# Optimization experiments

Measured on AMD Instinct MI355X. Metric: run time of the kernel, lower is better.

The kernel has to match this reference:

```python
import jax, jax.numpy as jnp
import numpy as np

DIM = 768      # d_model = d_inner (expand=1)
BSZ = 4
SEQ = 2048
DS  = 8        # d_state
DR  = 48       # dt_rank = ceil(768/16)
DC  = 4        # d_conv
EPS = 1e-5


def setup_inputs() -> dict:
    key = jax.random.key(0)
    ks = jax.random.split(key, 16)
    g = lambda k, shape, s=0.02: (jax.random.normal(k, shape, jnp.float32) * s)
    A_init = jnp.log(jnp.tile(jnp.arange(1, DS + 1, dtype=jnp.float32), (DIM, 1)))  # (D, N)
    return {
        "x": jax.random.normal(ks[0], (BSZ, SEQ, DIM), jnp.float32),
        "ln_g": jnp.ones((DIM,), jnp.float32),
        "ln_b": jnp.zeros((DIM,), jnp.float32),
        "in_proj_w": g(ks[1], (2 * DIM, DIM)),
        "conv_w": g(ks[2], (DIM, 1, DC), 0.2),
        "conv_b": jnp.zeros((DIM,), jnp.float32),
        "x_proj_w": g(ks[3], (DR + 2 * DS, DIM)),
        "dt_proj_w": g(ks[4], (DIM, DR), 0.1),
        "dt_proj_b": g(ks[5], (DIM,), 0.5) - 4.0,  # softplus -> small positive dt
        "A_log": A_init,
        "D": jnp.ones((DIM,), jnp.float32),
        "conv_w_b": g(ks[6], (DIM, 1, DC), 0.2),
        "conv_b_b": jnp.zeros((DIM,), jnp.float32),
        "x_proj_w_b": g(ks[7], (DR + 2 * DS, DIM)),
        "dt_proj_w_b": g(ks[8], (DIM, DR), 0.1),
        "dt_proj_b_b": g(ks[9], (DIM,), 0.5) - 4.0,
        "A_b_log": A_init,
        "D_b": jnp.ones((DIM,), jnp.float32),
        "out_proj_w": g(ks[10], (DIM, DIM)),
    }


def _ssm_dir(xl, zl, conv_w, conv_b, x_proj_w, dt_proj_w, dt_proj_b, A_log, Dp):
    # xl, zl: (B, L, D)
    d = xl.shape[-1]
    # causal depthwise conv along L (pad left d_conv-1)
    xc = jnp.pad(xl, ((0, 0), (DC - 1, 0), (0, 0))).transpose(0, 2, 1)  # (B, D, L+3)
    xconv = jax.lax.conv_general_dilated(
        xc, conv_w, (1,), "VALID", feature_group_count=d,
        dimension_numbers=("NCH", "OIH", "NCH"))  # (B, D, L)
    xs = jax.nn.silu(xconv + conv_b[None, :, None]).transpose(0, 2, 1)  # (B, L, D)
    x_dbl = xs @ x_proj_w.T                              # (B, L, R+2N)
    dt, Bm, Cm = jnp.split(x_dbl, [DR, DR + DS], axis=-1)
    delta = jax.nn.softplus(dt @ dt_proj_w.T + dt_proj_b)  # (B, L, D)
    A = -jnp.exp(A_log)                                  # (D, N)
    dA = jnp.exp(delta[..., None] * A)                   # (B, L, D, N)
    dBx = delta[..., None] * Bm[:, :, None, :] * xs[..., None]

    def comb(c1, c2):
        a1, b1 = c1
        a2, b2 = c2
        return (a2 * a1, a2 * b1 + b2)

    _, h = jax.lax.associative_scan(comb, (dA, dBx), axis=1)  # (B, L, D, N)
    y = jnp.einsum("bldn,bln->bld", h, Cm) + xs * Dp
    return y * jax.nn.silu(zl)


def _forward(x, ln_g, ln_b, in_proj_w, conv_w, conv_b, x_proj_w, dt_proj_w,
             dt_proj_b, A_log, D, conv_w_b, conv_b_b, x_proj_w_b, dt_proj_w_b,
             dt_proj_b_b, A_b_log, D_b, out_proj_w):
    mu = x.mean(-1, keepdims=True)
    var = ((x - mu) ** 2).mean(-1, keepdims=True)
    xn = (x - mu) * jax.lax.rsqrt(var + EPS) * ln_g + ln_b
    xz = xn @ in_proj_w.T                      # (B, L, 2D)
    xf, zf = jnp.split(xz, 2, axis=-1)
    # forward-direction scan
    yf = _ssm_dir(xf, zf, conv_w, conv_b, x_proj_w, dt_proj_w, dt_proj_b, A_log, D)
    # backward-direction scan (flip seq, scan, flip back) -- bimamba v2
    yb = _ssm_dir(xf[:, ::-1], zf[:, ::-1], conv_w_b, conv_b_b, x_proj_w_b,
                  dt_proj_w_b, dt_proj_b_b, A_b_log, D_b)[:, ::-1]
    out = ((yf + yb) * 0.5) @ out_proj_w.T     # if_devide_out=True
    return out + x                              # residual skip


def reference(x, ln_g, ln_b, in_proj_w, conv_w, conv_b, x_proj_w, dt_proj_w,
              dt_proj_b, A_log, D, conv_w_b, conv_b_b, x_proj_w_b, dt_proj_w_b,
              dt_proj_b_b, A_b_log, D_b, out_proj_w):
    return _forward(x, ln_g, ln_b, in_proj_w, conv_w, conv_b, x_proj_w,
                    dt_proj_w, dt_proj_b, A_log, D, conv_w_b, conv_b_b,
                    x_proj_w_b, dt_proj_w_b, dt_proj_b_b, A_b_log, D_b,
                    out_proj_w)
```

## Files before the change

### kernel.cpp

```cpp
#include <hip/hip_runtime.h>

#define Bsz 4
#define Lseq 2048
#define Dm 768
#define BL (Bsz * Lseq)
#define DS 8
#define DR 48
#define NCH 64
#define CHL 32
#define CW 32

typedef short bf16x8 __attribute__((ext_vector_type(8)));
typedef float f32x4 __attribute__((ext_vector_type(4)));
typedef float f32x2 __attribute__((ext_vector_type(2)));

typedef __attribute__((address_space(1))) const void gvoid_t;
typedef __attribute__((address_space(3))) void lvoid_t;
__device__ __forceinline__ void gll16(const void* g, void* l) {
    __builtin_amdgcn_global_load_lds((gvoid_t*)g, (lvoid_t*)l, 16, 0, 0);
}

__device__ __forceinline__ ushort f2bf(float f) {
    unsigned u = __builtin_bit_cast(unsigned, f);
    u += 0x7fff + ((u >> 16) & 1);
    return (ushort)(u >> 16);
}
__device__ __forceinline__ float bf2f(ushort u) {
    return __builtin_bit_cast(float, ((unsigned)u) << 16);
}
__device__ __forceinline__ float fsilu(float x) { return x / (1.f + __expf(-x)); }
__device__ __forceinline__ float fsoftplus(float x) {
    return fmaxf(x, 0.f) + __logf(1.f + __expf(-fabsf(x)));
}

#define PN0 (2 * Dm * Dm)
#define PN1 (Dm * Dm)
#define PN2 (64 * Dm)
#define PN5 (Dm * 64)
#define PREP_N (PN0 + PN1 + 2 * PN2 + 2 * PN5)
#define PREP_BLOCKS ((PREP_N + 255) / 256)

__global__ __launch_bounds__(256) void ln_prep_k(const float* __restrict__ x,
                                                 const float* __restrict__ g,
                                                 const float* __restrict__ bta,
                                                 ushort* __restrict__ xn,
                                                 const float* __restrict__ inW,
                                                 const float* __restrict__ outW,
                                                 const float* __restrict__ xpW,
                                                 const float* __restrict__ xpWb,
                                                 const float* __restrict__ dtw,
                                                 const float* __restrict__ dtwb,
                                                 ushort* __restrict__ w_in,
                                                 ushort* __restrict__ w_out,
                                                 ushort* __restrict__ w_xp,
                                                 ushort* __restrict__ w_xpb,
                                                 ushort* __restrict__ dtp,
                                                 ushort* __restrict__ dtpb) {
    if (blockIdx.x >= BL) {
        int i = (blockIdx.x - BL) * 256 + threadIdx.x;
        if (i < PN0) { w_in[i] = f2bf(inW[i]); return; }
        i -= PN0;
        if (i < PN1) { w_out[i] = f2bf(outW[i]); return; }
        i -= PN1;
        if (i < PN2) { w_xp[i] = f2bf(xpW[i]); return; }
        i -= PN2;
        if (i < PN2) { w_xpb[i] = f2bf(xpWb[i]); return; }
        i -= PN2;
        if (i < PN5) { int d = i >> 6, k = i & 63; dtp[i] = (k < DR) ? f2bf(dtw[d * DR + k]) : (ushort)0; return; }
        i -= PN5;
        if (i < PN5) { int d = i >> 6, k = i & 63; dtpb[i] = (k < DR) ? f2bf(dtwb[d * DR + k]) : (ushort)0; return; }
        return;
    }
    const int row = blockIdx.x, t = threadIdx.x;
    const float* xr = x + (size_t)row * Dm;
    float v0 = xr[t], v1 = xr[t + 256], v2 = xr[t + 512];
    float s1 = v0 + v1 + v2;
    float s2 = v0 * v0 + v1 * v1 + v2 * v2;
    for (int o = 32; o > 0; o >>= 1) { s1 += __shfl_down(s1, o); s2 += __shfl_down(s2, o); }
    __shared__ float r1[4], r2[4];
    int wv = t >> 6;
    if ((t & 63) == 0) { r1[wv] = s1; r2[wv] = s2; }
    __syncthreads();
    s1 = r1[0] + r1[1] + r1[2] + r1[3];
    s2 = r2[0] + r2[1] + r2[2] + r2[3];
    float mu = s1 * (1.f / Dm);
    float var = s2 * (1.f / Dm) - mu * mu;
    float rs = rsqrtf(var + 1e-5f);
    ushort* o = xn + (size_t)row * Dm;
    o[t]       = f2bf((v0 - mu) * rs * g[t]       + bta[t]);
    o[t + 256] = f2bf((v1 - mu) * rs * g[t + 256] + bta[t + 256]);
    o[t + 512] = f2bf((v2 - mu) * rs * g[t + 512] + bta[t + 512]);
}

template <int OUT_BF16, int ADD_RES>
__global__ __launch_bounds__(256) void gemm128(const ushort* __restrict__ A,
                                               const ushort* __restrict__ B,
                                               const float* __restrict__ res,
                                               void* __restrict__ Cout,
                                               int M, int N, int K) {
    __shared__ __align__(16) ushort lA[128 * 64];
    __shared__ __align__(16) ushort lB[128 * 64];
    const int t = threadIdx.x;
    const int nwgx = gridDim.x;
    const int nwg = nwgx * gridDim.y;
    const int orig = blockIdx.y * nwgx + blockIdx.x;
    const int cpx = nwg >> 3;
    const int swz = (orig & 7) * cpx + (orig >> 3);
    const int bm = swz % nwgx, bn = swz / nwgx;
    const int wave = t >> 6, lane = t & 63;
    const int wm = wave >> 1, wn = wave & 1;
    f32x4 acc[4][4] = {};

    const int lrow = lane >> 3;
    const int scol = ((lane & 7) ^ lrow) * 8;
    const int srow = wave * 32 + lrow;
    const ushort* gA = A + (size_t)(bm * 128 + srow) * K + scol;
    const ushort* gB = B + (size_t)(bn * 128 + srow) * K + scol;
    ushort* sA = &lA[srow * 64 + (lane & 7) * 8];
    ushort* sB = &lB[srow * 64 + (lane & 7) * 8];

    const int fr = lane & 15;
    const int fg = lane >> 4;
    const int rx = fr & 7;

    for (int k0 = 0; k0 < K; k0 += 64) {
#pragma unroll
        for (int j = 0; j < 4; j++) {
            gll16(gA + (size_t)(j * 8) * K, sA + j * 8 * 64);
            gll16(gB + (size_t)(j * 8) * K, sB + j * 8 * 64);
        }
        gA += 64; gB += 64;
        __syncthreads();
        bf16x8 af0[4], bf0[4], af1[4], bf1[4];
#pragma unroll
        for (int mi = 0; mi < 4; mi++) {
            int row = wm * 64 + mi * 16 + fr;
            af0[mi] = *(const bf16x8*)&lA[row * 64 + ((fg ^ rx) * 8)];
            af1[mi] = *(const bf16x8*)&lA[row * 64 + (((4 + fg) ^ rx) * 8)];
        }
#pragma unroll
        for (int ni = 0; ni < 4; ni++) {
            int row = wn * 64 + ni * 16 + fr;
            bf0[ni] = *(const bf16x8*)&lB[row * 64 + ((fg ^ rx) * 8)];
            bf1[ni] = *(const bf16x8*)&lB[row * 64 + (((4 + fg) ^ rx) * 8)];
        }
#pragma unroll
        for (int mi = 0; mi < 4; mi++)
#pragma unroll
            for (int ni = 0; ni < 4; ni++) {
                acc[mi][ni] = __builtin_amdgcn_mfma_f32_16x16x32_bf16(
                    af0[mi], bf0[ni], acc[mi][ni], 0, 0, 0);
                acc[mi][ni] = __builtin_amdgcn_mfma_f32_16x16x32_bf16(
                    af1[mi], bf1[ni], acc[mi][ni], 0, 0, 0);
            }
        __syncthreads();
    }
    const int rb = fg * 4;
#pragma unroll
    for (int mi = 0; mi < 4; mi++)
#pragma unroll
        for (int ni = 0; ni < 4; ni++) {
            int col = bn * 128 + wn * 64 + ni * 16 + fr;
#pragma unroll
            for (int r = 0; r < 4; r++) {
                int row = bm * 128 + wm * 64 + mi * 16 + rb + r;
                size_t o = (size_t)row * N + col;
                float v = acc[mi][ni][r];
                if (OUT_BF16) {
                    ((ushort*)Cout)[o] = f2bf(v);
                } else {
                    if (ADD_RES) v += res[o];
                    ((float*)Cout)[o] = v;
                }
            }
        }
}

__global__ __launch_bounds__(256) void gemm_dt(const ushort* __restrict__ A,
                                               const ushort* __restrict__ Bp0,
                                               const ushort* __restrict__ Bp1,
                                               const float* __restrict__ bias0,
                                               const float* __restrict__ bias1,
                                               ushort* __restrict__ delta) {
    __shared__ __align__(16) ushort lA[128 * 64];
    __shared__ __align__(16) ushort lB[128 * 64];
    const int t = threadIdx.x;
    const int nwgx = gridDim.x;
    const int nwg = nwgx * gridDim.y;
    const int orig = blockIdx.y * nwgx + blockIdx.x;
    const int cpx = nwg >> 3;
    const int swz = (orig & 7) * cpx + (orig >> 3);
    const int bm = swz % nwgx, bn = swz / nwgx;
    const ushort* __restrict__ B = (bm < BL / 128) ? Bp0 : Bp1;
    const float* __restrict__ bias = (bm < BL / 128) ? bias0 : bias1;
    const int wave = t >> 6, lane = t & 63;
    const int wm = wave >> 1, wn = wave & 1;
    f32x4 acc[4][4] = {};

    const int lrow = lane >> 3;
    const int scol = ((lane & 7) ^ lrow) * 8;
    const int srow = wave * 32 + lrow;
    const ushort* gA = A + (size_t)(bm * 128 + srow) * 64 + scol;
    const ushort* gB = B + (size_t)(bn * 128 + srow) * 64 + scol;
    ushort* sA = &lA[srow * 64 + (lane & 7) * 8];
    ushort* sB = &lB[srow * 64 + (lane & 7) * 8];

    const int fr = lane & 15;
    const int fg = lane >> 4;
    const int rx = fr & 7;

#pragma unroll
    for (int j = 0; j < 4; j++) {
        gll16(gA + (size_t)(j * 8) * 64, sA + j * 8 * 64);
        gll16(gB + (size_t)(j * 8) * 64, sB + j * 8 * 64);
    }
    __syncthreads();
    {
        bf16x8 af0[4], bf0[4], af1[4], bf1[4];
#pragma unroll
        for (int mi = 0; mi < 4; mi++) {
            int row = wm * 64 + mi * 16 + fr;
            af0[mi] = *(const bf16x8*)&lA[row * 64 + ((fg ^ rx) * 8)];
            af1[mi] = *(const bf16x8*)&lA[row * 64 + (((4 + fg) ^ rx) * 8)];
        }
#pragma unroll
        for (int ni = 0; ni < 4; ni++) {
            int row = wn * 64 + ni * 16 + fr;
            bf0[ni] = *(const bf16x8*)&lB[row * 64 + ((fg ^ rx) * 8)];
            bf1[ni] = *(const bf16x8*)&lB[row * 64 + (((4 + fg) ^ rx) * 8)];
        }
#pragma unroll
        for (int mi = 0; mi < 4; mi++)
#pragma unroll
            for (int ni = 0; ni < 4; ni++) {
                acc[mi][ni] = __builtin_amdgcn_mfma_f32_16x16x32_bf16(
                    af0[mi], bf0[ni], acc[mi][ni], 0, 0, 0);
                acc[mi][ni] = __builtin_amdgcn_mfma_f32_16x16x32_bf16(
                    af1[mi], bf1[ni], acc[mi][ni], 0, 0, 0);
            }
    }
    const int rb = fg * 4;
#pragma unroll
    for (int mi = 0; mi < 4; mi++)
#pragma unroll
        for (int ni = 0; ni < 4; ni++) {
            int col = bn * 128 + wn * 64 + ni * 16 + fr;
            float bv = bias[col];
#pragma unroll
            for (int r = 0; r < 4; r++) {
                int row = bm * 128 + wm * 64 + mi * 16 + rb + r;
                delta[(size_t)row * Dm + col] = f2bf(fsoftplus(acc[mi][ni][r] + bv));
            }
        }
}

__global__ __launch_bounds__(256) void gemm_xp2(const ushort* __restrict__ A,
                                                const ushort* __restrict__ B0,
                                                const ushort* __restrict__ B1,
                                                float* __restrict__ C,
                                                ushort* __restrict__ Cb) {
    __shared__ __align__(16) ushort lA[64 * 40];
    __shared__ __align__(16) ushort lB[64 * 40];
    const int t = threadIdx.x;
    const int bm = blockIdx.x;
    const ushort* __restrict__ B = (bm < BL / 64) ? B0 : B1;
    const int wave = t >> 6, lane = t & 63;
    const int wm = wave >> 1, wn = wave & 1;
    f32x4 acc[2][2] = {};

    const int srow = t >> 2;
    const int scol = (t & 3) << 3;
    const ushort* gA = A + (size_t)(bm * 64 + srow) * Dm + scol;
    const ushort* gB = B + (size_t)srow * Dm + scol;
    ushort* sA = &lA[srow * 40 + scol];
    ushort* sB = &lB[srow * 40 + scol];
    const int fra = wm * 32 + (lane & 15);
    const int frb = wn * 32 + (lane & 15);
    const int fk = (lane >> 4) << 3;

    for (int k0 = 0; k0 < Dm; k0 += 32) {
        *(uint4*)sA = *(const uint4*)gA;
        *(uint4*)sB = *(const uint4*)gB;
        gA += 32; gB += 32;
        __syncthreads();
        bf16x8 a0 = *(const bf16x8*)&lA[fra * 40 + fk];
        bf16x8 a1 = *(const bf16x8*)&lA[(fra + 16) * 40 + fk];
        bf16x8 b0 = *(const bf16x8*)&lB[frb * 40 + fk];
        bf16x8 b1 = *(const bf16x8*)&lB[(frb + 16) * 40 + fk];
        acc[0][0] = __builtin_amdgcn_mfma_f32_16x16x32_bf16(a0, b0, acc[0][0], 0, 0, 0);
        acc[0][1] = __builtin_amdgcn_mfma_f32_16x16x32_bf16(a0, b1, acc[0][1], 0, 0, 0);
        acc[1][0] = __builtin_amdgcn_mfma_f32_16x16x32_bf16(a1, b0, acc[1][0], 0, 0, 0);
        acc[1][1] = __builtin_amdgcn_mfma_f32_16x16x32_bf16(a1, b1, acc[1][1], 0, 0, 0);
        __syncthreads();
    }
    const int rb = (lane >> 4) << 2;
    for (int mi = 0; mi < 2; mi++)
        for (int ni = 0; ni < 2; ni++) {
            int col = wn * 32 + ni * 16 + (lane & 15);
            for (int r = 0; r < 4; r++) {
                int row = bm * 64 + wm * 32 + mi * 16 + rb + r;
                float v = acc[mi][ni][r];
                C[(size_t)row * 64 + col] = v;
                Cb[(size_t)row * 64 + col] = f2bf(v);
            }
        }
}

__global__ __launch_bounds__(256) void conv_silu2_k(const ushort* __restrict__ xzb,
                                                    const float* __restrict__ cwf,
                                                    const float* __restrict__ cbf,
                                                    const float* __restrict__ cwb,
                                                    const float* __restrict__ cbb,
                                                    ushort* __restrict__ xs_bf) {
    const int d = blockIdx.x * 256 + threadIdx.x;
    const int w = blockIdx.y * CW;
    const int b = blockIdx.z;
    const ushort* xcol = xzb + (size_t)b * Lseq * (2 * Dm) + d;
    const float wf0 = cwf[d * 4 + 0], wf1 = cwf[d * 4 + 1],
                wf2 = cwf[d * 4 + 2], wf3 = cwf[d * 4 + 3];
    const float wb0 = cwb[d * 4 + 0], wb1 = cwb[d * 4 + 1],
                wb2 = cwb[d * 4 + 2], wb3 = cwb[d * 4 + 3];
    const float bfv = cbf[d], bbv = cbb[d];
    float x0 = 0.f, x1 = 0.f, x2 = 0.f, x3 = 0.f;
#pragma unroll
    for (int s = 0; s < CW + 6; ++s) {
        int i = w - 3 + s;
        x0 = x1; x1 = x2; x2 = x3;
        x3 = (i >= 0 && i < Lseq) ? bf2f(xcol[(size_t)i * (2 * Dm)]) : 0.f;
        if (i >= w && i < w + CW) {
            float a = bfv + wf0 * x0 + wf1 * x1 + wf2 * x2 + wf3 * x3;
            xs_bf[((size_t)b * Lseq + i) * Dm + d] = f2bf(fsilu(a));
        }
        int q = i - 3;
        if (q >= w && q < w + CW) {
            float a = bbv + wb0 * x3 + wb1 * x2 + wb2 * x1 + wb3 * x0;
            int j = Lseq - 1 - q;
            xs_bf[((size_t)BL + (size_t)b * Lseq + j) * Dm + d] = f2bf(fsilu(a));
        }
    }
}

__global__ __launch_bounds__(256) void scanA2_k(const ushort* __restrict__ delta,
                                                const ushort* __restrict__ xs_bf,
                                                const float* __restrict__ xdbl,
                                                float* __restrict__ agg_a,
                                                float* __restrict__ agg_h) {
    __shared__ __align__(16) float sB[CHL][8];
    const int t = threadIdx.x;
    int d = blockIdx.x * 256 + t;
    int chunk = blockIdx.y;
    int zz = blockIdx.z;
    int dir = zz >> 2, b = zz & 3;
    size_t rowbase = (size_t)dir * BL + (size_t)b * Lseq + (size_t)chunk * CHL;
    {
        int rr = t >> 3, cc = t & 7;
        sB[rr][cc] = xdbl[(rowbase + rr) * 64 + DR + cc];
    }
    __syncthreads();
    f32x2 h01 = {0.f, 0.f}, h23 = {0.f, 0.f}, h45 = {0.f, 0.f}, h67 = {0.f, 0.f};
    float sumdlt = 0.f;
    size_t r = rowbase;
    for (int l = 0; l < CHL; l++) {
        float dlt = bf2f(delta[r * Dm + d]);
        float xv = bf2f(xs_bf[r * Dm + d]);
        const float4* p = (const float4*)sB[l];
        float4 bA = p[0], bB = p[1];
        float dx = dlt * xv;
        sumdlt += dlt;
        float e1 = __expf(-dlt);
        float e2 = e1 * e1;
        f32x2 e2p = {e2, e2};
        f32x2 dA01 = {e1, e2};
        f32x2 dA23 = dA01 * e2p;
        f32x2 dA45 = dA23 * e2p;
        f32x2 dA67 = dA45 * e2p;
        f32x2 dx2 = {dx, dx};
        f32x2 vb01 = {bA.x, bA.y}, vb23 = {bA.z, bA.w};
        f32x2 vb45 = {bB.x, bB.y}, vb67 = {bB.z, bB.w};
        h01 = dA01 * h01 + dx2 * vb01;
        h23 = dA23 * h23 + dx2 * vb23;
        h45 = dA45 * h45 + dx2 * vb45;
        h67 = dA67 * h67 + dx2 * vb67;
        r++;
    }
    float E1 = __expf(-sumdlt);
    float E2 = E1 * E1;
    f32x2 E2p = {E2, E2};
    f32x2 P01 = {E1, E2};
    f32x2 P23 = P01 * E2p;
    f32x2 P45 = P23 * E2p;
    f32x2 P67 = P45 * E2p;
    size_t o = (((size_t)(dir * Bsz + b) * NCH + chunk) * Dm + d) * DS;
    float4 pa0 = {P01.x, P01.y, P23.x, P23.y};
    float4 pa1 = {P45.x, P45.y, P67.x, P67.y};
    float4 ph0 = {h01.x, h01.y, h23.x, h23.y};
    float4 ph1 = {h45.x, h45.y, h67.x, h67.y};
    *(float4*)(agg_a + o) = pa0;
    *(float4*)(agg_a + o + 4) = pa1;
    *(float4*)(agg_h + o) = ph0;
    *(float4*)(agg_h + o + 4) = ph1;
}

__global__ __launch_bounds__(256) void scanB2_k(const float* __restrict__ agg_a,
                                                float* __restrict__ agg_h) {
    int idx = blockIdx.x * 256 + threadIdx.x;
    if (idx >= 2 * Bsz * Dm * DS) return;
    const int DSM = Dm * DS;
    int bb = idx / DSM;
    int rem = idx - bb * DSM;
    size_t base = (size_t)bb * NCH * DSM + rem;
    float h = 0.f;
#pragma unroll 4
    for (int c = 0; c < NCH; c++) {
        size_t a = base + (size_t)c * DSM;
        float ga = agg_a[a], gh = agg_h[a];
        agg_h[a] = h;
        h = ga * h + gh;
    }
}

__global__ __launch_bounds__(256) void scanCM_k(const ushort* __restrict__ delta,
                                                const ushort* __restrict__ xs_bf,
                                                const float* __restrict__ xdbl,
                                                const float* __restrict__ D0,
                                                const float* __restrict__ D1,
                                                const float* __restrict__ hinit,
                                                const ushort* __restrict__ xzb,
                                                ushort* __restrict__ ybf) {
    __shared__ __align__(16) float sBCf[CHL][16];
    __shared__ __align__(16) float sBCb[CHL][16];
    const int t = threadIdx.x;
    int d = blockIdx.x * 256 + t;
    int chunk = blockIdx.y;
    int b = blockIdx.z;
    int cb = NCH - 1 - chunk;
    size_t rbf = (size_t)b * Lseq + (size_t)chunk * CHL;
    size_t rbb = (size_t)BL + (size_t)b * Lseq + (size_t)cb * CHL;
    {
        int rr = t >> 3, cc = (t & 7) * 2;
        const float* sf = xdbl + (rbf + rr) * 64 + DR + cc;
        sBCf[rr][cc] = sf[0];
        sBCf[rr][cc + 1] = sf[1];
        const float* sb = xdbl + (rbb + rr) * 64 + DR + cc;
        sBCb[rr][cc] = sb[0];
        sBCb[rr][cc + 1] = sb[1];
    }
    __syncthreads();

    float yf_arr[CHL];
    {
        size_t hb = (((size_t)b * NCH + chunk) * Dm + d) * DS;
        float4 hA = ((const float4*)(hinit + hb))[0];
        float4 hB = ((const float4*)(hinit + hb))[1];
        f32x2 h01 = {hA.x, hA.y}, h23 = {hA.z, hA.w};
        f32x2 h45 = {hB.x, hB.y}, h67 = {hB.z, hB.w};
        float Dv = D0[d];
#pragma unroll
        for (int l = 0; l < CHL; l++) {
            size_t r = rbf + l;
            float dlt = bf2f(delta[r * Dm + d]);
            float xv = bf2f(xs_bf[r * Dm + d]);
            const float4* p = (const float4*)sBCf[l];
            float4 bA = p[0], bB = p[1], cA = p[2], cB = p[3];
            float dx = dlt * xv;
            float e1 = __expf(-dlt);
            float e2 = e1 * e1;
            f32x2 e2p = {e2, e2};
            f32x2 dA01 = {e1, e2};
            f32x2 dA23 = dA01 * e2p;
            f32x2 dA45 = dA23 * e2p;
            f32x2 dA67 = dA45 * e2p;
            f32x2 dx2 = {dx, dx};
            f32x2 vb01 = {bA.x, bA.y}, vb23 = {bA.z, bA.w};
            f32x2 vb45 = {bB.x, bB.y}, vb67 = {bB.z, bB.w};
            f32x2 vc01 = {cA.x, cA.y}, vc23 = {cA.z, cA.w};
            f32x2 vc45 = {cB.x, cB.y}, vc67 = {cB.z, cB.w};
            h01 = dA01 * h01 + dx2 * vb01;
            h23 = dA23 * h23 + dx2 * vb23;
            h45 = dA45 * h45 + dx2 * vb45;
            h67 = dA67 * h67 + dx2 * vb67;
            f32x2 yv = h01 * vc01;
            yv = h23 * vc23 + yv;
            yv = h45 * vc45 + yv;
            yv = h67 * vc67 + yv;
            yf_arr[l] = fmaf(xv, Dv, yv.x + yv.y);
        }
    }
    {
        size_t hb = (((size_t)(Bsz + b) * NCH + cb) * Dm + d) * DS;
        float4 hA = ((const float4*)(hinit + hb))[0];
        float4 hB = ((const float4*)(hinit + hb))[1];
        f32x2 h01 = {hA.x, hA.y}, h23 = {hA.z, hA.w};
        f32x2 h45 = {hB.x, hB.y}, h67 = {hB.z, hB.w};
        float Dv = D1[d];
#pragma unroll
        for (int lp = 0; lp < CHL; lp++) {
            size_t r = rbb + lp;
            float dlt = bf2f(delta[r * Dm + d]);
            float xv = bf2f(xs_bf[r * Dm + d]);
            const float4* p = (const float4*)sBCb[lp];
            float4 bA = p[0], bB = p[1], cA = p[2], cB = p[3];
            float dx = dlt * xv;
            float e1 = __expf(-dlt);
            float e2 = e1 * e1;
            f32x2 e2p = {e2, e2};
            f32x2 dA01 = {e1, e2};
            f32x2 dA23 = dA01 * e2p;
            f32x2 dA45 = dA23 * e2p;
            f32x2 dA67 = dA45 * e2p;
            f32x2 dx2 = {dx, dx};
            f32x2 vb01 = {bA.x, bA.y}, vb23 = {bA.z, bA.w};
            f32x2 vb45 = {bB.x, bB.y}, vb67 = {bB.z, bB.w};
            f32x2 vc01 = {cA.x, cA.y}, vc23 = {cA.z, cA.w};
            f32x2 vc45 = {cB.x, cB.y}, vc67 = {cB.z, cB.w};
            h01 = dA01 * h01 + dx2 * vb01;
            h23 = dA23 * h23 + dx2 * vb23;
            h45 = dA45 * h45 + dx2 * vb45;
            h67 = dA67 * h67 + dx2 * vb67;
            f32x2 yv = h01 * vc01;
            yv = h23 * vc23 + yv;
            yv = h45 * vc45 + yv;
            yv = h67 * vc67 + yv;
            float yb = fmaf(xv, Dv, yv.x + yv.y);
            int q = chunk * CHL + (CHL - 1 - lp);
            float yf = yf_arr[CHL - 1 - lp];
            float z = bf2f(xzb[((size_t)b * Lseq + q) * (2 * Dm) + Dm + d]);
            ybf[((size_t)b * Lseq + q) * Dm + d] = f2bf(0.5f * (yf + yb) * fsilu(z));
        }
    }
}

extern "C" void kernel_launch(void* const* d_in, const int* in_sizes, int n_in,
                              void* d_out, int out_size, void* d_ws, size_t ws_size,
                              hipStream_t stream) {
    const float* x        = (const float*)d_in[0];
    const float* ln_g     = (const float*)d_in[1];
    const float* ln_b     = (const float*)d_in[2];
    const float* in_proj  = (const float*)d_in[3];
    const float* conv_w   = (const float*)d_in[4];
    const float* conv_b   = (const float*)d_in[5];
    const float* xproj_w  = (const float*)d_in[6];
    const float* dtw      = (const float*)d_in[7];
    const float* dtb      = (const float*)d_in[8];
    const float* Dvec     = (const float*)d_in[10];
    const float* conv_w_b = (const float*)d_in[11];
    const float* conv_b_b = (const float*)d_in[12];
    const float* xproj_w_b= (const float*)d_in[13];
    const float* dtw_b    = (const float*)d_in[14];
    const float* dtb_b    = (const float*)d_in[15];
    const float* Dvec_b   = (const float*)d_in[17];
    const float* outproj  = (const float*)d_in[18];
    float* out = (float*)d_out;

    char* p = (char*)d_ws;
    auto alloc = [&](size_t bytes) {
        char* r = p;
        p += (bytes + 255) & ~(size_t)255;
        return r;
    };
    ushort* w_in_bf  = (ushort*)alloc((size_t)2 * Dm * Dm * 2);
    ushort* w_out_bf = (ushort*)alloc((size_t)Dm * Dm * 2);
    ushort* w_xp_bf  = (ushort*)alloc((size_t)64 * Dm * 2);
    ushort* w_xpb_bf = (ushort*)alloc((size_t)64 * Dm * 2);
    ushort* dtwp_f   = (ushort*)alloc((size_t)Dm * 64 * 2);
    ushort* dtwp_b   = (ushort*)alloc((size_t)Dm * 64 * 2);
    ushort* xn_bf    = (ushort*)alloc((size_t)BL * Dm * 2);
    ushort* xz_bf    = (ushort*)alloc((size_t)BL * 2 * Dm * 2);
    ushort* xs_bf2   = (ushort*)alloc((size_t)(2 * BL + 8) * Dm * 2);
    float*  xdbl2    = (float*)alloc((size_t)(2 * BL + 8) * 64 * 4);
    ushort* xdblb    = (ushort*)alloc((size_t)2 * BL * 64 * 2);
    ushort* delta2   = (ushort*)alloc((size_t)(2 * BL + 8) * Dm * 2);
    float*  agg_a2   = (float*)alloc((size_t)2 * Bsz * Dm * NCH * DS * 4);
    float*  agg_h2   = (float*)alloc((size_t)2 * Bsz * Dm * NCH * DS * 4);
    ushort* ybf      = xn_bf;

    ln_prep_k<<<BL + PREP_BLOCKS, 256, 0, stream>>>(
        x, ln_g, ln_b, xn_bf,
        in_proj, outproj, xproj_w, xproj_w_b, dtw, dtw_b,
        w_in_bf, w_out_bf, w_xp_bf, w_xpb_bf, dtwp_f, dtwp_b);

    gemm128<1, 0><<<dim3(BL / 128, (2 * Dm) / 128), 256, 0, stream>>>(
        xn_bf, w_in_bf, nullptr, xz_bf, BL, 2 * Dm, Dm);

    conv_silu2_k<<<dim3(3, Lseq / CW, Bsz), 256, 0, stream>>>(
        xz_bf, conv_w, conv_b, conv_w_b, conv_b_b, xs_bf2);
    gemm_xp2<<<dim3(2 * BL / 64, 1), 256, 0, stream>>>(
        xs_bf2, w_xp_bf, w_xpb_bf, xdbl2, xdblb);
    gemm_dt<<<dim3(2 * BL / 128, Dm / 128), 256, 0, stream>>>(
        xdblb, dtwp_f, dtwp_b, dtb, dtb_b, delta2);
    scanA2_k<<<dim3(3, NCH, 2 * Bsz), 256, 0, stream>>>(
        delta2, xs_bf2, xdbl2, agg_a2, agg_h2);
    scanB2_k<<<(2 * Bsz * Dm * DS + 255) / 256, 256, 0, stream>>>(agg_a2, agg_h2);
    scanCM_k<<<dim3(3, NCH, Bsz), 256, 0, stream>>>(
        delta2, xs_bf2, xdbl2, Dvec, Dvec_b, agg_h2, xz_bf, ybf);

    gemm128<0, 1><<<dim3(BL / 128, Dm / 128), 256, 0, stream>>>(
        ybf, w_out_bf, x, out, BL, Dm, Dm);
}
```

Baseline: 159.9 us.

## Fuse causal depthwise conv and SiLU into the x_proj GEMM A-tile load

Removes the separate conv_silu kernel. The x_proj GEMM now computes the 4-tap depthwise conv plus SiLU for both scan directions while it stages the A tile into LDS, and also writes the xs result for later kernels. Conv weights and bias are pre-transposed to bf16 in the prep kernel so they can be loaded as vectors. This saves one launch and a read of xs. In exchange each GEMM block reads four input rows per element, and conv weights are now rounded to bf16, which slightly changes numerics.

```diff
diff --git a/kernel.cpp b/kernel.cpp
--- a/kernel.cpp
+++ b/kernel.cpp
@@ -8,7 +8,6 @@
 #define DR 48
 #define NCH 64
 #define CHL 32
-#define CW 32
 
 typedef short bf16x8 __attribute__((ext_vector_type(8)));
 typedef float f32x4 __attribute__((ext_vector_type(4)));
@@ -37,7 +36,9 @@
 #define PN1 (Dm * Dm)
 #define PN2 (64 * Dm)
 #define PN5 (Dm * 64)
-#define PREP_N (PN0 + PN1 + 2 * PN2 + 2 * PN5)
+#define PN6 (4 * Dm)
+#define PN7 (Dm)
+#define PREP_N (PN0 + PN1 + 2 * PN2 + 2 * PN5 + 2 * PN6 + 2 * PN7)
 #define PREP_BLOCKS ((PREP_N + 255) / 256)
 
 __global__ __launch_bounds__(256) void ln_prep_k(const float* __restrict__ x,
@@ -50,12 +51,20 @@
                                                  const float* __restrict__ xpWb,
                                                  const float* __restrict__ dtw,
                                                  const float* __restrict__ dtwb,
+                                                 const float* __restrict__ cw0,
+                                                 const float* __restrict__ cb0,
+                                                 const float* __restrict__ cw1,
+                                                 const float* __restrict__ cb1,
                                                  ushort* __restrict__ w_in,
                                                  ushort* __restrict__ w_out,
                                                  ushort* __restrict__ w_xp,
                                                  ushort* __restrict__ w_xpb,
                                                  ushort* __restrict__ dtp,
-                                                 ushort* __restrict__ dtpb) {
+                                                 ushort* __restrict__ dtpb,
+                                                 ushort* __restrict__ cwt0,
+                                                 ushort* __restrict__ cbt0,
+                                                 ushort* __restrict__ cwt1,
+                                                 ushort* __restrict__ cbt1) {
     if (blockIdx.x >= BL) {
         int i = (blockIdx.x - BL) * 256 + threadIdx.x;
         if (i < PN0) { w_in[i] = f2bf(inW[i]); return; }
@@ -69,6 +78,14 @@
         if (i < PN5) { int d = i >> 6, k = i & 63; dtp[i] = (k < DR) ? f2bf(dtw[d * DR + k]) : (ushort)0; return; }
         i -= PN5;
         if (i < PN5) { int d = i >> 6, k = i & 63; dtpb[i] = (k < DR) ? f2bf(dtwb[d * DR + k]) : (ushort)0; return; }
+        i -= PN5;
+        if (i < PN6) { int k = i / Dm, ch = i - k * Dm; cwt0[i] = f2bf(cw0[ch * 4 + k]); return; }
+        i -= PN6;
+        if (i < PN6) { int k = i / Dm, ch = i - k * Dm; cwt1[i] = f2bf(cw1[ch * 4 + k]); return; }
+        i -= PN6;
+        if (i < PN7) { cbt0[i] = f2bf(cb0[i]); return; }
+        i -= PN7;
+        if (i < PN7) { cbt1[i] = f2bf(cb1[i]); return; }
         return;
     }
     const int row = blockIdx.x, t = threadIdx.x;
@@ -254,23 +271,35 @@
         }
 }
 
-__global__ __launch_bounds__(256) void gemm_xp2(const ushort* __restrict__ A,
-                                                const ushort* __restrict__ B0,
-                                                const ushort* __restrict__ B1,
-                                                float* __restrict__ C,
-                                                ushort* __restrict__ Cb) {
+__global__ __launch_bounds__(256) void conv_xp2_k(const ushort* __restrict__ xzb,
+                                                  const ushort* __restrict__ B0,
+                                                  const ushort* __restrict__ B1,
+                                                  const ushort* __restrict__ cwt0,
+                                                  const ushort* __restrict__ cbt0,
+                                                  const ushort* __restrict__ cwt1,
+                                                  const ushort* __restrict__ cbt1,
+                                                  ushort* __restrict__ xs_bf,
+                                                  float* __restrict__ C,
+                                                  ushort* __restrict__ Cb) {
     __shared__ __align__(16) ushort lA[64 * 40];
     __shared__ __align__(16) ushort lB[64 * 40];
     const int t = threadIdx.x;
     const int bm = blockIdx.x;
-    const ushort* __restrict__ B = (bm < BL / 64) ? B0 : B1;
+    const int fwd = (bm < BL / 64);
+    const ushort* __restrict__ B = fwd ? B0 : B1;
+    const ushort* __restrict__ cwt = fwd ? cwt0 : cwt1;
+    const ushort* __restrict__ cbt = fwd ? cbt0 : cbt1;
+    const int rloc = (fwd ? bm : bm - BL / 64) * 64;
+    const int b = rloc / Lseq;
+    const int srow = t >> 2;
+    const int l = (rloc % Lseq) + srow;
+    const int scol = (t & 3) << 3;
+    const ushort* __restrict__ xb = xzb + (size_t)b * Lseq * (2 * Dm);
+    ushort* __restrict__ xsrow = xs_bf + ((size_t)(fwd ? 0 : BL) + rloc + srow) * Dm;
+
     const int wave = t >> 6, lane = t & 63;
     const int wm = wave >> 1, wn = wave & 1;
     f32x4 acc[2][2] = {};
-
-    const int srow = t >> 2;
-    const int scol = (t & 3) << 3;
-    const ushort* gA = A + (size_t)(bm * 64 + srow) * Dm + scol;
     const ushort* gB = B + (size_t)srow * Dm + scol;
     ushort* sA = &lA[srow * 40 + scol];
     ushort* sB = &lB[srow * 40 + scol];
@@ -279,9 +308,37 @@
     const int fk = (lane >> 4) << 3;
 
     for (int k0 = 0; k0 < Dm; k0 += 32) {
-        *(uint4*)sA = *(const uint4*)gA;
+        const int ch = k0 + scol;
+        float o[8];
+        {
+            uint4 ub = *(const uint4*)(cbt + ch);
+            const ushort* s = (const ushort*)&ub;
+#pragma unroll
+            for (int j = 0; j < 8; j++) o[j] = bf2f(s[j]);
+        }
+#pragma unroll
+        for (int k = 0; k < 4; k++) {
+            int src = fwd ? (l - 3 + k) : (Lseq + 2 - l - k);
+            uint4 uw = *(const uint4*)(cwt + k * Dm + ch);
+            const ushort* sw = (const ushort*)&uw;
+            if ((unsigned)src < (unsigned)Lseq) {
+                uint4 ux = *(const uint4*)(xb + (size_t)src * (2 * Dm) + ch);
+                const ushort* sx = (const ushort*)&ux;
+#pragma unroll
+                for (int j = 0; j < 8; j++)
+                    o[j] = fmaf(bf2f(sw[j]), bf2f(sx[j]), o[j]);
+            }
+        }
+        uint4 pk;
+        {
+            ushort* ps = (ushort*)&pk;
+#pragma unroll
+            for (int j = 0; j < 8; j++) ps[j] = f2bf(fsilu(o[j]));
+        }
+        *(uint4*)sA = pk;
+        *(uint4*)(xsrow + ch) = pk;
         *(uint4*)sB = *(const uint4*)gB;
-        gA += 32; gB += 32;
+        gB += 32;
         __syncthreads();
         bf16x8 a0 = *(const bf16x8*)&lA[fra * 40 + fk];
         bf16x8 a1 = *(const bf16x8*)&lA[(fra + 16) * 40 + fk];
@@ -304,40 +361,6 @@
                 Cb[(size_t)row * 64 + col] = f2bf(v);
             }
         }
-}
-
-__global__ __launch_bounds__(256) void conv_silu2_k(const ushort* __restrict__ xzb,
-                                                    const float* __restrict__ cwf,
-                                                    const float* __restrict__ cbf,
-                                                    const float* __restrict__ cwb,
-                                                    const float* __restrict__ cbb,
-                                                    ushort* __restrict__ xs_bf) {
-    const int d = blockIdx.x * 256 + threadIdx.x;
-    const int w = blockIdx.y * CW;
-    const int b = blockIdx.z;
-    const ushort* xcol = xzb + (size_t)b * Lseq * (2 * Dm) + d;
-    const float wf0 = cwf[d * 4 + 0], wf1 = cwf[d * 4 + 1],
-                wf2 = cwf[d * 4 + 2], wf3 = cwf[d * 4 + 3];
-    const float wb0 = cwb[d * 4 + 0], wb1 = cwb[d * 4 + 1],
-                wb2 = cwb[d * 4 + 2], wb3 = cwb[d * 4 + 3];
-    const float bfv = cbf[d], bbv = cbb[d];
-    float x0 = 0.f, x1 = 0.f, x2 = 0.f, x3 = 0.f;
-#pragma unroll
-    for (int s = 0; s < CW + 6; ++s) {
-        int i = w - 3 + s;
-        x0 = x1; x1 = x2; x2 = x3;
-        x3 = (i >= 0 && i < Lseq) ? bf2f(xcol[(size_t)i * (2 * Dm)]) : 0.f;
-        if (i >= w && i < w + CW) {
-            float a = bfv + wf0 * x0 + wf1 * x1 + wf2 * x2 + wf3 * x3;
-            xs_bf[((size_t)b * Lseq + i) * Dm + d] = f2bf(fsilu(a));
-        }
-        int q = i - 3;
-        if (q >= w && q < w + CW) {
-            float a = bbv + wb0 * x3 + wb1 * x2 + wb2 * x1 + wb3 * x0;
-            int j = Lseq - 1 - q;
-            xs_bf[((size_t)BL + (size_t)b * Lseq + j) * Dm + d] = f2bf(fsilu(a));
-        }
-    }
 }
 
 __global__ __launch_bounds__(256) void scanA2_k(const ushort* __restrict__ delta,
@@ -564,6 +587,10 @@
     ushort* w_xpb_bf = (ushort*)alloc((size_t)64 * Dm * 2);
     ushort* dtwp_f   = (ushort*)alloc((size_t)Dm * 64 * 2);
     ushort* dtwp_b   = (ushort*)alloc((size_t)Dm * 64 * 2);
+    ushort* cwt_f    = (ushort*)alloc((size_t)4 * Dm * 2);
+    ushort* cbt_f    = (ushort*)alloc((size_t)Dm * 2);
+    ushort* cwt_b    = (ushort*)alloc((size_t)4 * Dm * 2);
+    ushort* cbt_b    = (ushort*)alloc((size_t)Dm * 2);
     ushort* xn_bf    = (ushort*)alloc((size_t)BL * Dm * 2);
     ushort* xz_bf    = (ushort*)alloc((size_t)BL * 2 * Dm * 2);
     ushort* xs_bf2   = (ushort*)alloc((size_t)(2 * BL + 8) * Dm * 2);
@@ -577,15 +604,17 @@
     ln_prep_k<<<BL + PREP_BLOCKS, 256, 0, stream>>>(
         x, ln_g, ln_b, xn_bf,
         in_proj, outproj, xproj_w, xproj_w_b, dtw, dtw_b,
-        w_in_bf, w_out_bf, w_xp_bf, w_xpb_bf, dtwp_f, dtwp_b);
+        conv_w, conv_b, conv_w_b, conv_b_b,
+        w_in_bf, w_out_bf, w_xp_bf, w_xpb_bf, dtwp_f, dtwp_b,
+        cwt_f, cbt_f, cwt_b, cbt_b);
 
     gemm128<1, 0><<<dim3(BL / 128, (2 * Dm) / 128), 256, 0, stream>>>(
         xn_bf, w_in_bf, nullptr, xz_bf, BL, 2 * Dm, Dm);
 
-    conv_silu2_k<<<dim3(3, Lseq / CW, Bsz), 256, 0, stream>>>(
-        xz_bf, conv_w, conv_b, conv_w_b, conv_b_b, xs_bf2);
-    gemm_xp2<<<dim3(2 * BL / 64, 1), 256, 0, stream>>>(
-        xs_bf2, w_xp_bf, w_xpb_bf, xdbl2, xdblb);
+    conv_xp2_k<<<dim3(2 * BL / 64, 1), 256, 0, stream>>>(
+        xz_bf, w_xp_bf, w_xpb_bf, cwt_f, cbt_f, cwt_b, cbt_b,
+        xs_bf2, xdbl2, xdblb);
+
     gemm_dt<<<dim3(2 * BL / 128, Dm / 128), 256, 0, stream>>>(
         xdblb, dtwp_f, dtwp_b, dtb, dtb_b, delta2);
     scanA2_k<<<dim3(3, NCH, 2 * Bsz), 256, 0, stream>>>(
```

Result: slower. 181.2 us (+13.3%).
